# Performance work log

Measured on AMD Instinct MI355X. Metric: run time of the kernel, lower is better.

The kernel has to match this reference:

```python
import jax, jax.numpy as jnp
import numpy as np

N = 100_000
E = 1_600_000
IN_F, E_F, OUT_F = 32, 16, 32


def _glorot(key, shape):
    lim = np.sqrt(6.0 / (shape[0] + shape[1])).astype(np.float32)
    return jax.random.uniform(key, shape, jnp.float32, -lim, lim)


def setup_inputs() -> dict:
    key = jax.random.key(0)
    ks = jax.random.split(key, 12)
    return {
        'h_feat': jax.random.normal(ks[0], (N, IN_F), jnp.float32),
        'e_feat': jax.random.normal(ks[1], (N, E_F), jnp.float32),
        'rain0': jax.random.normal(ks[2], (N,), jnp.float32),
        'w_xx': jax.random.uniform(ks[3], (E,), jnp.float32),
        'w_yy': jax.random.uniform(ks[4], (E,), jnp.float32),
        'W_trans': _glorot(ks[5], (E_F + IN_F, OUT_F)),            # transform_h (no bias)
        'W_rin': _glorot(ks[6], (OUT_F + 4 * E_F, 4 * OUT_F)),     # Rainfall_in (no bias)
        'W_rout': _glorot(ks[7], (4 * OUT_F, 1)),                  # Rainfall_out (no bias)
        'src_xx': jax.random.randint(ks[8], (E,), 0, N, jnp.int32),
        'dst_xx': jax.random.randint(ks[9], (E,), 0, N, jnp.int32),
        'src_yy': jax.random.randint(ks[10], (E,), 0, N, jnp.int32),
        'dst_yy': jax.random.randint(ks[11], (E,), 0, N, jnp.int32),
    }


def _segsum(msg, dst):
    return jax.ops.segment_sum(msg, dst, num_segments=N)


def reference(h_feat, e_feat, rain0, w_xx, w_yy, W_trans, W_rin, W_rout,
              src_xx, dst_xx, src_yy, dst_yy):
    # node-wise transform: cat(h, e) -> linear -> activation_edge (relu)
    emh = jax.nn.relu(jnp.concatenate([h_feat, e_feat], axis=1) @ W_trans)  # [N, OUT_F]
    # copy_u + sum over both edge types, then activation (relu)
    h = jax.nn.relu(_segsum(emh[src_xx], dst_xx) + _segsum(emh[src_yy], dst_yy))
    # first-order weighted differences of e_feat, scattered to dst
    grad_x = _segsum(w_xx[:, None] * (e_feat[src_xx] - e_feat[dst_xx]), dst_xx)  # [N, E_F]
    grad_y = _segsum(w_yy[:, None] * (e_feat[src_yy] - e_feat[dst_yy]), dst_yy)
    # second-order weighted differences
    grad_2x = _segsum(w_xx[:, None] * (grad_x[src_xx] - grad_x[dst_xx]), dst_xx)
    grad_2y = _segsum(w_yy[:, None] * (grad_y[src_yy] - grad_y[dst_yy]), dst_yy)
    h_cat = jnp.concatenate([h, grad_x, grad_y, grad_2x, grad_2y], axis=1)  # [N, OUT_F+4*E_F]
    rain_h = jax.nn.relu(h_cat @ W_rin)
    rainfall = rain0[:, None] + rain_h @ W_rout  # error_mode=True
    return rainfall, h
```

## Files before the change

kernel.cpp:

```cpp
#include <hip/hip_runtime.h>
#include <hip/hip_bf16.h>

#define NN 100000
#define EE 1600000
#define SCAN_CHUNK 4096
#define NB ((NN + SCAN_CHUNK - 1) / SCAN_CHUNK)
#define OFFP (NN + 8)
#define NRANGE 4
#define RSZ (NN / NRANGE)
#define C_CH 16
#define CHUNK_E (EE / C_CH)
#define AP 104

typedef __attribute__((ext_vector_type(8))) short bf16x8;
typedef __attribute__((ext_vector_type(4))) float f32x4;

__device__ inline unsigned short f2bf(float f) {
    unsigned u = __float_as_uint(f);
    return (unsigned short)((u + 0x7FFFu + ((u >> 16) & 1u)) >> 16);
}
__device__ inline float bf2f(unsigned short u) {
    return __uint_as_float(((unsigned)u) << 16);
}

__global__ __launch_bounds__(1024) void fused_th_k(const float* __restrict__ h_feat,
                                                   const float* __restrict__ e_feat,
                                                   const float* __restrict__ W_trans,
                                                   unsigned short* __restrict__ emh_bf,
                                                   unsigned short* __restrict__ ef_bf,
                                                   const int* __restrict__ dst_a,
                                                   const int* __restrict__ dst_b,
                                                   int* __restrict__ partial, int TB) {
    __shared__ float Wl[48 * 32];
    __shared__ int bins[RSZ];
    if ((int)blockIdx.x < TB) {
        for (int i = threadIdx.x; i < 48 * 32; i += 1024) Wl[i] = W_trans[i];
        __syncthreads();
        int t = blockIdx.x * 1024 + threadIdx.x;
        if (t >= NN * 32) return;
        int n = t >> 5, j = t & 31;
        const float* hrow = h_feat + (size_t)n * 32;
        const float* erow = e_feat + (size_t)n * 16;
        float acc = 0.f;
#pragma unroll 8
        for (int k = 0; k < 32; ++k) acc = fmaf(hrow[k], Wl[k * 32 + j], acc);
#pragma unroll 8
        for (int k = 0; k < 16; ++k) acc = fmaf(erow[k], Wl[(32 + k) * 32 + j], acc);
        emh_bf[t] = f2bf(fmaxf(acc, 0.f));
        if (j < 16) ef_bf[(size_t)n * 16 + j] = f2bf(erow[j]);
    } else {
        for (int i = threadIdx.x; i < RSZ; i += 1024) bins[i] = 0;
        __syncthreads();
        const int idx = (int)blockIdx.x - TB;
        const int q = idx & 7;
        const int t = q >> 2;
        const int p = q & 3;
        const int c = idx >> 3;
        const int* dst = t ? dst_b : dst_a;
        const int lo = p * RSZ;
        const long base = (long)c * CHUNK_E;
        for (int i = threadIdx.x * 4; i < CHUNK_E; i += 4096) {
            int4 d = *reinterpret_cast<const int4*>(dst + base + i);
            int x;
            x = d.x - lo; if ((unsigned)x < RSZ) atomicAdd(&bins[x], 1);
            x = d.y - lo; if ((unsigned)x < RSZ) atomicAdd(&bins[x], 1);
            x = d.z - lo; if ((unsigned)x < RSZ) atomicAdd(&bins[x], 1);
            x = d.w - lo; if ((unsigned)x < RSZ) atomicAdd(&bins[x], 1);
        }
        __syncthreads();
        int* pout = partial + (long)(t * C_CH + c) * NN + lo;
        for (int i = threadIdx.x; i < RSZ; i += 1024) pout[i] = bins[i];
    }
}

__global__ __launch_bounds__(1024) void scanA_k(const int* __restrict__ partial,
                                                int* __restrict__ bsum) {
    __shared__ int wsum[16];
    const int b = blockIdx.x;
    const int t = (b >= NB) ? 1 : 0;
    const int i0 = (b % NB) * SCAN_CHUNK + threadIdx.x * 4;
    int4 s = make_int4(0, 0, 0, 0);
    if (i0 < NN) {
#pragma unroll
        for (int c = 0; c < C_CH; ++c) {
            int4 v = *reinterpret_cast<const int4*>(partial + (long)(t * C_CH + c) * NN + i0);
            s.x += v.x; s.y += v.y; s.z += v.z; s.w += v.w;
        }
    }
    int tot = s.x + s.y + s.z + s.w;
#pragma unroll
    for (int d = 32; d; d >>= 1) tot += __shfl_down(tot, d);
    int lane = threadIdx.x & 63, w = threadIdx.x >> 6;
    if (lane == 0) wsum[w] = tot;
    __syncthreads();
    if (threadIdx.x == 0) {
        int sm = 0;
#pragma unroll
        for (int q = 0; q < 16; ++q) sm += wsum[q];
        bsum[b] = sm;
    }
}

__global__ __launch_bounds__(64) void scanB_k(const int* __restrict__ bsum,
                                              int* __restrict__ bbase,
                                              int* __restrict__ off_a,
                                              int* __restrict__ off_b) {
    int lane = threadIdx.x;
    int v = (lane < 2 * NB) ? bsum[lane] : 0;
    int seg = lane / NB;
    int inc = v;
#pragma unroll
    for (int d = 1; d < 64; d <<= 1) {
        int x = __shfl_up(inc, d);
        if (lane >= d && (lane - d) / NB == seg) inc += x;
    }
    int excl = inc - v;
    if (lane < 2 * NB) bbase[lane] = excl;
    if (lane == NB - 1) off_a[NN] = inc;
    if (lane == 2 * NB - 1) off_b[NN] = inc;
}

__global__ __launch_bounds__(1024) void scanC_k(int* __restrict__ partial,
                                                int* __restrict__ off_a,
                                                int* __restrict__ off_b,
                                                const int* __restrict__ bbase) {
    __shared__ int wsum[16];
    const int b = blockIdx.x;
    const int t = (b >= NB) ? 1 : 0;
    int* off = t ? off_b : off_a;
    const int base0 = bbase[b];
    const int i0 = (b % NB) * SCAN_CHUNK + threadIdx.x * 4;
    int4 s = make_int4(0, 0, 0, 0);
    if (i0 < NN) {
#pragma unroll
        for (int c = 0; c < C_CH; ++c) {
            int4 v = *reinterpret_cast<const int4*>(partial + (long)(t * C_CH + c) * NN + i0);
            s.x += v.x; s.y += v.y; s.z += v.z; s.w += v.w;
        }
    }
    int s1 = s.x, s2 = s1 + s.y, s3 = s2 + s.z, tot = s3 + s.w;
    int lane = threadIdx.x & 63, w = threadIdx.x >> 6;
    int inc = tot;
#pragma unroll
    for (int d = 1; d < 64; d <<= 1) {
        int x = __shfl_up(inc, d);
        if (lane >= d) inc += x;
    }
    if (lane == 63) wsum[w] = inc;
    int texcl = inc - tot;
    __syncthreads();
    if (threadIdx.x == 0) {
        int r = 0;
#pragma unroll
        for (int q = 0; q < 16; ++q) { int x = wsum[q]; wsum[q] = r; r += x; }
    }
    __syncthreads();
    const int base = base0 + wsum[w] + texcl;
    if (i0 < NN) {
        *reinterpret_cast<int4*>(off + i0) = make_int4(base, base + s1, base + s2, base + s3);
        int4 run = make_int4(base, base + s1, base + s2, base + s3);
#pragma unroll
        for (int c = 0; c < C_CH; ++c) {
            int* p = partial + (long)(t * C_CH + c) * NN + i0;
            int4 v = *reinterpret_cast<const int4*>(p);
            *reinterpret_cast<int4*>(p) = run;
            run.x += v.x; run.y += v.y; run.z += v.z; run.w += v.w;
        }
    }
}

__global__ __launch_bounds__(1024) void scatter_k(const int* __restrict__ dst_a,
                                                  const int* __restrict__ src_a,
                                                  const float* __restrict__ w_a,
                                                  const int* __restrict__ dst_b,
                                                  const int* __restrict__ src_b,
                                                  const float* __restrict__ w_b,
                                                  const int* __restrict__ partial,
                                                  int2* __restrict__ csr_a,
                                                  int2* __restrict__ csr_b) {
    __shared__ int curs[RSZ];
    const int bid = blockIdx.x;
    const int q = bid & 7;
    const int t = q >> 2;
    const int p = q & 3;
    const int c = bid >> 3;
    const int* dst = t ? dst_b : dst_a;
    const int* src = t ? src_b : src_a;
    const float* wv = t ? w_b : w_a;
    int2* csr = t ? csr_b : csr_a;
    const int lo = p * RSZ;
    const int* pin = partial + (long)(t * C_CH + c) * NN + lo;
    for (int i = threadIdx.x; i < RSZ; i += 1024) curs[i] = pin[i];
    __syncthreads();
    const long base = (long)c * CHUNK_E;
    for (int i = threadIdx.x * 4; i < CHUNK_E; i += 4096) {
        int4 d = *reinterpret_cast<const int4*>(dst + base + i);
        int4 s = *reinterpret_cast<const int4*>(src + base + i);
        float4 w = *reinterpret_cast<const float4*>(wv + base + i);
        int x;
        x = d.x - lo;
        if ((unsigned)x < RSZ) {
            int pp = atomicAdd(&curs[x], 1);
            csr[pp] = make_int2(s.x, __float_as_int(w.x));
        }
        x = d.y - lo;
        if ((unsigned)x < RSZ) {
            int pp = atomicAdd(&curs[x], 1);
            csr[pp] = make_int2(s.y, __float_as_int(w.y));
        }
        x = d.z - lo;
        if ((unsigned)x < RSZ) {
            int pp = atomicAdd(&curs[x], 1);
            csr[pp] = make_int2(s.z, __float_as_int(w.z));
        }
        x = d.w - lo;
        if ((unsigned)x < RSZ) {
            int pp = atomicAdd(&curs[x], 1);
            csr[pp] = make_int2(s.w, __float_as_int(w.w));
        }
    }
}

__global__ __launch_bounds__(256) void pull1_k(const unsigned short* __restrict__ emh_bf,
                                               const unsigned short* __restrict__ ef_bf,
                                               const float* __restrict__ e_feat,
                                               const int2* __restrict__ csr_a,
                                               const int* __restrict__ off_a,
                                               const int2* __restrict__ csr_b,
                                               const int* __restrict__ off_b,
                                               float* __restrict__ out_h,
                                               float* __restrict__ gx,
                                               float* __restrict__ gy,
                                               unsigned short* __restrict__ gx_bf,
                                               unsigned short* __restrict__ gy_bf) {
    int g = blockIdx.x * 256 + threadIdx.x;
    int n = g >> 5, j = g & 31;
    if (n >= NN) return;
    float acc_h = 0.f;

#pragma unroll
    for (int half = 0; half < 2; ++half) {
        const int2* csr = half ? csr_b : csr_a;
        const int* off = half ? off_b : off_a;
        float* gout = half ? gy : gx;
        unsigned short* gbf = half ? gy_bf : gx_bf;
        float acc_g = 0.f, sumw = 0.f;
        int k = off[n], e2 = off[n + 1];
        for (; k + 3 < e2; k += 4) {
            int2 s0 = csr[k], s1 = csr[k + 1], s2 = csr[k + 2], s3 = csr[k + 3];
            float m0 = bf2f(emh_bf[(size_t)s0.x * 32 + j]);
            float m1 = bf2f(emh_bf[(size_t)s1.x * 32 + j]);
            float m2 = bf2f(emh_bf[(size_t)s2.x * 32 + j]);
            float m3 = bf2f(emh_bf[(size_t)s3.x * 32 + j]);
            acc_h += (m0 + m1) + (m2 + m3);
            if (j < 16) {
                float w0 = __int_as_float(s0.y), w1 = __int_as_float(s1.y);
                float w2 = __int_as_float(s2.y), w3 = __int_as_float(s3.y);
                acc_g = fmaf(w0, bf2f(ef_bf[(size_t)s0.x * 16 + j]), acc_g);
                acc_g = fmaf(w1, bf2f(ef_bf[(size_t)s1.x * 16 + j]), acc_g);
                acc_g = fmaf(w2, bf2f(ef_bf[(size_t)s2.x * 16 + j]), acc_g);
                acc_g = fmaf(w3, bf2f(ef_bf[(size_t)s3.x * 16 + j]), acc_g);
                sumw += (w0 + w1) + (w2 + w3);
            }
        }
        for (; k < e2; ++k) {
            int2 s0 = csr[k];
            acc_h += bf2f(emh_bf[(size_t)s0.x * 32 + j]);
            if (j < 16) {
                float w0 = __int_as_float(s0.y);
                acc_g = fmaf(w0, bf2f(ef_bf[(size_t)s0.x * 16 + j]), acc_g);
                sumw += w0;
            }
        }
        if (j < 16) {
            float val = acc_g - sumw * e_feat[(size_t)n * 16 + j];
            gout[(size_t)n * 16 + j] = val;
            gbf[(size_t)n * 16 + j] = f2bf(val);
        }
    }
    out_h[(size_t)n * 32 + j] = fmaxf(acc_h, 0.f);
}

__global__ __launch_bounds__(256) void pull2_k(const float* __restrict__ gx,
                                               const float* __restrict__ gy,
                                               const unsigned short* __restrict__ gx_bf,
                                               const unsigned short* __restrict__ gy_bf,
                                               const int2* __restrict__ csr_a,
                                               const int* __restrict__ off_a,
                                               const int2* __restrict__ csr_b,
                                               const int* __restrict__ off_b,
                                               float* __restrict__ g2x,
                                               float* __restrict__ g2y) {
    int g = blockIdx.x * 256 + threadIdx.x;
    int n = g >> 4, j = g & 15;
    if (n >= NN) return;

#pragma unroll
    for (int half = 0; half < 2; ++half) {
        const int2* csr = half ? csr_b : csr_a;
        const int* off = half ? off_b : off_a;
        const float* gin = half ? gy : gx;
        const unsigned short* gbf = half ? gy_bf : gx_bf;
        float* g2 = half ? g2y : g2x;
        float acc = 0.f, sumw = 0.f;
        int k = off[n], e2 = off[n + 1];
        for (; k + 3 < e2; k += 4) {
            int2 s0 = csr[k], s1 = csr[k + 1], s2 = csr[k + 2], s3 = csr[k + 3];
            float w0 = __int_as_float(s0.y), w1 = __int_as_float(s1.y);
            float w2 = __int_as_float(s2.y), w3 = __int_as_float(s3.y);
            acc = fmaf(w0, bf2f(gbf[(size_t)s0.x * 16 + j]), acc);
            acc = fmaf(w1, bf2f(gbf[(size_t)s1.x * 16 + j]), acc);
            acc = fmaf(w2, bf2f(gbf[(size_t)s2.x * 16 + j]), acc);
            acc = fmaf(w3, bf2f(gbf[(size_t)s3.x * 16 + j]), acc);
            sumw += (w0 + w1) + (w2 + w3);
        }
        for (; k < e2; ++k) {
            int2 s0 = csr[k];
            float w0 = __int_as_float(s0.y);
            acc = fmaf(w0, bf2f(gbf[(size_t)s0.x * 16 + j]), acc);
            sumw += w0;
        }
        g2[(size_t)n * 16 + j] = acc - sumw * gin[(size_t)n * 16 + j];
    }
}

__global__ __launch_bounds__(256) void final_mfma_k(const float* __restrict__ h,
                                                    const float* __restrict__ gx,
                                                    const float* __restrict__ gy,
                                                    const float* __restrict__ g2x,
                                                    const float* __restrict__ g2y,
                                                    const float* __restrict__ rain0,
                                                    const float* __restrict__ W_rin,
                                                    const float* __restrict__ W_rout,
                                                    float* __restrict__ out_rain) {
    __shared__ __align__(16) unsigned short Wt[128 * AP];
    __shared__ __align__(16) unsigned short At[64 * AP];
    __shared__ float Wo[128];
    const int tid = threadIdx.x;

    for (int i = tid; i < 3072; i += 256) {
        int k = i >> 5;
        int c = (i & 31) * 4;
        float4 wv = *reinterpret_cast<const float4*>(W_rin + k * 128 + c);
        Wt[(c + 0) * AP + k] = f2bf(wv.x);
        Wt[(c + 1) * AP + k] = f2bf(wv.y);
        Wt[(c + 2) * AP + k] = f2bf(wv.z);
        Wt[(c + 3) * AP + k] = f2bf(wv.w);
    }
    if (tid < 128) Wo[tid] = W_rout[tid];

    {
        int n = tid >> 2, q = tid & 3;
        int node = blockIdx.x * 64 + n;
        float f[24];
#define LD4(di, p) { float4 v_ = *reinterpret_cast<const float4*>(p); \
                     f[di] = v_.x; f[di+1] = v_.y; f[di+2] = v_.z; f[di+3] = v_.w; }
        if (node < NN) {
            if (q == 0) {
                LD4(0,  h + (size_t)node * 32 + 0);
                LD4(4,  h + (size_t)node * 32 + 4);
                LD4(8,  h + (size_t)node * 32 + 8);
                LD4(12, h + (size_t)node * 32 + 12);
                LD4(16, h + (size_t)node * 32 + 16);
                LD4(20, h + (size_t)node * 32 + 20);
            } else if (q == 1) {
                LD4(0,  h + (size_t)node * 32 + 24);
                LD4(4,  h + (size_t)node * 32 + 28);
                LD4(8,  gx + (size_t)node * 16 + 0);
                LD4(12, gx + (size_t)node * 16 + 4);
                LD4(16, gx + (size_t)node * 16 + 8);
                LD4(20, gx + (size_t)node * 16 + 12);
            } else if (q == 2) {
                LD4(0,  gy + (size_t)node * 16 + 0);
                LD4(4,  gy + (size_t)node * 16 + 4);
                LD4(8,  gy + (size_t)node * 16 + 8);
                LD4(12, gy + (size_t)node * 16 + 12);
                LD4(16, g2x + (size_t)node * 16 + 0);
                LD4(20, g2x + (size_t)node * 16 + 4);
            } else {
                LD4(0,  g2x + (size_t)node * 16 + 8);
                LD4(4,  g2x + (size_t)node * 16 + 12);
                LD4(8,  g2y + (size_t)node * 16 + 0);
                LD4(12, g2y + (size_t)node * 16 + 4);
                LD4(16, g2y + (size_t)node * 16 + 8);
                LD4(20, g2y + (size_t)node * 16 + 12);
            }
        } else {
#pragma unroll
            for (int i = 0; i < 24; ++i) f[i] = 0.f;
        }
#undef LD4
        unsigned pk[12];
#pragma unroll
        for (int i = 0; i < 12; ++i)
            pk[i] = (unsigned)f2bf(f[2 * i]) | ((unsigned)f2bf(f[2 * i + 1]) << 16);
        char* dp = (char*)At + n * (AP * 2) + q * 48;
        *reinterpret_cast<uint4*>(dp + 0)  = make_uint4(pk[0], pk[1], pk[2], pk[3]);
        *reinterpret_cast<uint4*>(dp + 16) = make_uint4(pk[4], pk[5], pk[6], pk[7]);
        *reinterpret_cast<uint4*>(dp + 32) = make_uint4(pk[8], pk[9], pk[10], pk[11]);
    }
    __syncthreads();

    const int w = tid >> 6;
    const int l = tid & 63;
    const int col = l & 15;
    const int kg = l >> 4;
    const char* Ab = (const char*)At + (w * 16 + col) * (AP * 2) + kg * 16;
    const char* Bb = (const char*)Wt + col * (AP * 2) + kg * 16;

    f32x4 acc[8];
#pragma unroll
    for (int ct = 0; ct < 8; ++ct) acc[ct] = (f32x4){0.f, 0.f, 0.f, 0.f};

#pragma unroll
    for (int ks = 0; ks < 3; ++ks) {
        bf16x8 af = *reinterpret_cast<const bf16x8*>(Ab + ks * 64);
#pragma unroll
        for (int ct = 0; ct < 8; ++ct) {
            bf16x8 bfr = *reinterpret_cast<const bf16x8*>(Bb + ct * 16 * (AP * 2) + ks * 64);
            acc[ct] = __builtin_amdgcn_mfma_f32_16x16x32_bf16(af, bfr, acc[ct], 0, 0, 0);
        }
    }

    float s0 = 0.f, s1 = 0.f, s2 = 0.f, s3 = 0.f;
#pragma unroll
    for (int ct = 0; ct < 8; ++ct) {
        float wo = Wo[ct * 16 + col];
        s0 = fmaf(fmaxf(acc[ct][0], 0.f), wo, s0);
        s1 = fmaf(fmaxf(acc[ct][1], 0.f), wo, s1);
        s2 = fmaf(fmaxf(acc[ct][2], 0.f), wo, s2);
        s3 = fmaf(fmaxf(acc[ct][3], 0.f), wo, s3);
    }
#pragma unroll
    for (int m = 1; m < 16; m <<= 1) {
        s0 += __shfl_xor(s0, m);
        s1 += __shfl_xor(s1, m);
        s2 += __shfl_xor(s2, m);
        s3 += __shfl_xor(s3, m);
    }
    if (col == 0) {
        int row = blockIdx.x * 64 + w * 16 + kg * 4;
        if (row + 0 < NN) out_rain[row + 0] = rain0[row + 0] + s0;
        if (row + 1 < NN) out_rain[row + 1] = rain0[row + 1] + s1;
        if (row + 2 < NN) out_rain[row + 2] = rain0[row + 2] + s2;
        if (row + 3 < NN) out_rain[row + 3] = rain0[row + 3] + s3;
    }
}

extern "C" void kernel_launch(void* const* d_in, const int* in_sizes, int n_in,
                              void* d_out, int out_size, void* d_ws, size_t ws_size,
                              hipStream_t stream) {
    const float* h_feat  = (const float*)d_in[0];
    const float* e_feat  = (const float*)d_in[1];
    const float* rain0   = (const float*)d_in[2];
    const float* w_xx    = (const float*)d_in[3];
    const float* w_yy    = (const float*)d_in[4];
    const float* W_trans = (const float*)d_in[5];
    const float* W_rin   = (const float*)d_in[6];
    const float* W_rout  = (const float*)d_in[7];
    const int* src_xx    = (const int*)d_in[8];
    const int* dst_xx    = (const int*)d_in[9];
    const int* src_yy    = (const int*)d_in[10];
    const int* dst_yy    = (const int*)d_in[11];

    unsigned short* emh_bf = (unsigned short*)d_ws;
    unsigned short* ef_bf  = emh_bf + (size_t)NN * 32;
    unsigned short* gx_bf  = ef_bf + (size_t)NN * 16;
    unsigned short* gy_bf  = gx_bf + (size_t)NN * 16;
    float* gx = (float*)(gy_bf + (size_t)NN * 16);
    float* gy = gx + (size_t)NN * 16;
    int2* csr_xx = (int2*)(gy + (size_t)NN * 16);
    int2* csr_yy = csr_xx + EE;
    int* off_xx  = (int*)(csr_yy + EE);
    int* off_yy  = off_xx + OFFP;
    int* partial = off_yy + OFFP;
    float* g2x   = (float*)partial;
    float* g2y   = g2x + (size_t)NN * 16;
    int* bsum    = partial + (size_t)2 * C_CH * NN;
    int* bbase   = bsum + 64;

    float* out_rain = (float*)d_out;
    float* out_h    = out_rain + NN;

    const int TB = (NN * 32 + 1023) / 1024;
    const int HB = 2 * NRANGE * C_CH;
    fused_th_k<<<TB + HB, 1024, 0, stream>>>(h_feat, e_feat, W_trans, emh_bf, ef_bf,
                                             dst_xx, dst_yy, partial, TB);

    scanA_k<<<2 * NB, 1024, 0, stream>>>(partial, bsum);
    scanB_k<<<1, 64, 0, stream>>>(bsum, bbase, off_xx, off_yy);
    scanC_k<<<2 * NB, 1024, 0, stream>>>(partial, off_xx, off_yy, bbase);

    scatter_k<<<2 * NRANGE * C_CH, 1024, 0, stream>>>(
        dst_xx, src_xx, w_xx, dst_yy, src_yy, w_yy, partial, csr_xx, csr_yy);

    pull1_k<<<(NN * 32 + 255) / 256, 256, 0, stream>>>(
        emh_bf, ef_bf, e_feat, csr_xx, off_xx, csr_yy, off_yy,
        out_h, gx, gy, gx_bf, gy_bf);

    pull2_k<<<(NN * 16 + 255) / 256, 256, 0, stream>>>(
        gx, gy, gx_bf, gy_bf, csr_xx, off_xx, csr_yy, off_yy, g2x, g2y);

    final_mfma_k<<<(NN + 63) / 64, 256, 0, stream>>>(
        out_h, gx, gy, g2x, g2y, rain0, W_rin, W_rout, out_rain);
}
```

Before: 301.5 us.

## Replace range-filtered CSR scatter with two-pass bucketed radix partition

Builds the CSR with a two-pass bucket sort. A new count kernel histograms destinations into 1024-node buckets per chunk, a small prefix kernel derives per-chunk bucket cursors, a partition kernel writes packed (src, local dst, weight) records into an intermediate buffer, and a per-bucket kernel scatters them into the final CSR using shared-memory cursors. The old scatter had every block scan its whole chunk four times, once per destination range, and write to scattered global positions. The new scheme reads each edge once per pass and keeps the final scatter local to each bucket. The cost is an extra intermediate buffer, two more launches, and an extra read and write of the edge records. Packing the source index into 20 bits relies on N being below about 1M.

```diff
diff --git a/kernel.cpp b/kernel.cpp
--- a/kernel.cpp
+++ b/kernel.cpp
@@ -10,6 +10,10 @@
 #define RSZ (NN / NRANGE)
 #define C_CH 16
 #define CHUNK_E (EE / C_CH)
+#define BS 1024
+#define NBUK ((NN + BS - 1) / BS)
+#define P_CH 128
+#define PCHUNK_E (EE / P_CH)
 #define AP 104
 
 typedef __attribute__((ext_vector_type(8))) short bf16x8;
@@ -120,7 +124,7 @@
     if (lane == 2 * NB - 1) off_b[NN] = inc;
 }
 
-__global__ __launch_bounds__(1024) void scanC_k(int* __restrict__ partial,
+__global__ __launch_bounds__(1024) void scanC_k(const int* __restrict__ partial,
                                                 int* __restrict__ off_a,
                                                 int* __restrict__ off_b,
                                                 const int* __restrict__ bbase) {
@@ -156,68 +160,111 @@
     }
     __syncthreads();
     const int base = base0 + wsum[w] + texcl;
-    if (i0 < NN) {
+    if (i0 < NN)
         *reinterpret_cast<int4*>(off + i0) = make_int4(base, base + s1, base + s2, base + s3);
-        int4 run = make_int4(base, base + s1, base + s2, base + s3);
-#pragma unroll
-        for (int c = 0; c < C_CH; ++c) {
-            int* p = partial + (long)(t * C_CH + c) * NN + i0;
-            int4 v = *reinterpret_cast<const int4*>(p);
-            *reinterpret_cast<int4*>(p) = run;
-            run.x += v.x; run.y += v.y; run.z += v.z; run.w += v.w;
-        }
-    }
-}
-
-__global__ __launch_bounds__(1024) void scatter_k(const int* __restrict__ dst_a,
-                                                  const int* __restrict__ src_a,
-                                                  const float* __restrict__ w_a,
-                                                  const int* __restrict__ dst_b,
-                                                  const int* __restrict__ src_b,
-                                                  const float* __restrict__ w_b,
-                                                  const int* __restrict__ partial,
-                                                  int2* __restrict__ csr_a,
-                                                  int2* __restrict__ csr_b) {
-    __shared__ int curs[RSZ];
-    const int bid = blockIdx.x;
-    const int q = bid & 7;
-    const int t = q >> 2;
-    const int p = q & 3;
-    const int c = bid >> 3;
+}
+
+__global__ __launch_bounds__(256) void count2_k(const int* __restrict__ dst_a,
+                                                const int* __restrict__ dst_b,
+                                                int* __restrict__ count2) {
+    __shared__ int bins[NBUK];
+    for (int i = threadIdx.x; i < NBUK; i += 256) bins[i] = 0;
+    __syncthreads();
+    const int t = blockIdx.x >> 7;
+    const int c = blockIdx.x & 127;
+    const int* dst = t ? dst_b : dst_a;
+    const long base = (long)c * PCHUNK_E;
+    for (int i = threadIdx.x * 4; i < PCHUNK_E; i += 1024) {
+        int4 d = *reinterpret_cast<const int4*>(dst + base + i);
+        atomicAdd(&bins[d.x >> 10], 1);
+        atomicAdd(&bins[d.y >> 10], 1);
+        atomicAdd(&bins[d.z >> 10], 1);
+        atomicAdd(&bins[d.w >> 10], 1);
+    }
+    __syncthreads();
+    int* out = count2 + ((long)t * P_CH + c) * NBUK;
+    for (int i = threadIdx.x; i < NBUK; i += 256) out[i] = bins[i];
+}
+
+__global__ __launch_bounds__(256) void cur2_k(const int* __restrict__ count2,
+                                              const int* __restrict__ off_a,
+                                              const int* __restrict__ off_b,
+                                              int* __restrict__ cur2) {
+    int tid = threadIdx.x;
+    if (tid >= 2 * NBUK) return;
+    int t = tid / NBUK;
+    int b = tid % NBUK;
+    const int* off = t ? off_b : off_a;
+    int run = off[b * BS];
+    for (int c = 0; c < P_CH; ++c) {
+        long idx = ((long)t * P_CH + c) * NBUK + b;
+        int v = count2[idx];
+        cur2[idx] = run;
+        run += v;
+    }
+}
+
+__global__ __launch_bounds__(1024) void part_k(const int* __restrict__ dst_a,
+                                               const int* __restrict__ src_a,
+                                               const float* __restrict__ w_a,
+                                               const int* __restrict__ dst_b,
+                                               const int* __restrict__ src_b,
+                                               const float* __restrict__ w_b,
+                                               const int* __restrict__ cur2,
+                                               int2* __restrict__ inter_a,
+                                               int2* __restrict__ inter_b) {
+    __shared__ int lcur[NBUK];
+    const int t = blockIdx.x >> 7;
+    const int c = blockIdx.x & 127;
     const int* dst = t ? dst_b : dst_a;
     const int* src = t ? src_b : src_a;
     const float* wv = t ? w_b : w_a;
-    int2* csr = t ? csr_b : csr_a;
-    const int lo = p * RSZ;
-    const int* pin = partial + (long)(t * C_CH + c) * NN + lo;
-    for (int i = threadIdx.x; i < RSZ; i += 1024) curs[i] = pin[i];
-    __syncthreads();
-    const long base = (long)c * CHUNK_E;
-    for (int i = threadIdx.x * 4; i < CHUNK_E; i += 4096) {
+    int2* inter = t ? inter_b : inter_a;
+    {
+        const int* cin = cur2 + ((long)t * P_CH + c) * NBUK;
+        for (int i = threadIdx.x; i < NBUK; i += 1024) lcur[i] = cin[i];
+    }
+    __syncthreads();
+    const long base = (long)c * PCHUNK_E;
+    for (int i = threadIdx.x * 4; i < PCHUNK_E; i += 4096) {
         int4 d = *reinterpret_cast<const int4*>(dst + base + i);
         int4 s = *reinterpret_cast<const int4*>(src + base + i);
         float4 w = *reinterpret_cast<const float4*>(wv + base + i);
-        int x;
-        x = d.x - lo;
-        if ((unsigned)x < RSZ) {
-            int pp = atomicAdd(&curs[x], 1);
-            csr[pp] = make_int2(s.x, __float_as_int(w.x));
-        }
-        x = d.y - lo;
-        if ((unsigned)x < RSZ) {
-            int pp = atomicAdd(&curs[x], 1);
-            csr[pp] = make_int2(s.y, __float_as_int(w.y));
-        }
-        x = d.z - lo;
-        if ((unsigned)x < RSZ) {
-            int pp = atomicAdd(&curs[x], 1);
-            csr[pp] = make_int2(s.z, __float_as_int(w.z));
-        }
-        x = d.w - lo;
-        if ((unsigned)x < RSZ) {
-            int pp = atomicAdd(&curs[x], 1);
-            csr[pp] = make_int2(s.w, __float_as_int(w.w));
-        }
+        int pos;
+        pos = atomicAdd(&lcur[d.x >> 10], 1);
+        inter[pos] = make_int2(s.x | ((d.x & 1023) << 20), __float_as_int(w.x));
+        pos = atomicAdd(&lcur[d.y >> 10], 1);
+        inter[pos] = make_int2(s.y | ((d.y & 1023) << 20), __float_as_int(w.y));
+        pos = atomicAdd(&lcur[d.z >> 10], 1);
+        inter[pos] = make_int2(s.z | ((d.z & 1023) << 20), __float_as_int(w.z));
+        pos = atomicAdd(&lcur[d.w >> 10], 1);
+        inter[pos] = make_int2(s.w | ((d.w & 1023) << 20), __float_as_int(w.w));
+    }
+}
+
+__global__ __launch_bounds__(1024) void scat2_k(const int2* __restrict__ inter_a,
+                                                const int2* __restrict__ inter_b,
+                                                const int* __restrict__ off_a,
+                                                const int* __restrict__ off_b,
+                                                int2* __restrict__ csr_a,
+                                                int2* __restrict__ csr_b) {
+    __shared__ int curs[BS];
+    const int t = ((int)blockIdx.x >= NBUK) ? 1 : 0;
+    const int b = (int)blockIdx.x - t * NBUK;
+    const int2* inter = t ? inter_b : inter_a;
+    const int* off = t ? off_b : off_a;
+    int2* csr = t ? csr_b : csr_a;
+    const int n0 = b * BS;
+    const int nend = (n0 + BS < NN) ? n0 + BS : NN;
+    for (int i = threadIdx.x; i < nend - n0; i += 1024) curs[i] = off[n0 + i];
+    __syncthreads();
+    const int lo = off[n0];
+    const int hi = off[nend];
+    for (int i = lo + threadIdx.x; i < hi; i += 1024) {
+        int2 e = inter[i];
+        int dloc = (e.x >> 20) & 1023;
+        int pos = atomicAdd(&curs[dloc], 1);
+        csr[pos] = make_int2(e.x & 0xFFFFF, e.y);
     }
 }
 
@@ -474,10 +521,15 @@
     int* off_xx  = (int*)(csr_yy + EE);
     int* off_yy  = off_xx + OFFP;
     int* partial = off_yy + OFFP;
-    float* g2x   = (float*)partial;
+    int2* inter_xx = (int2*)partial;
+    int2* inter_yy = inter_xx + EE;
+    float* g2x   = (float*)inter_xx;
     float* g2y   = g2x + (size_t)NN * 16;
-    int* bsum    = partial + (size_t)2 * C_CH * NN;
+    int* tail    = (int*)(inter_yy + EE);
+    int* bsum    = tail;
     int* bbase   = bsum + 64;
+    int* count2  = bbase + 64;
+    int* cur2    = count2 + 2 * P_CH * NBUK;
 
     float* out_rain = (float*)d_out;
     float* out_h    = out_rain + NN;
@@ -491,8 +543,14 @@
     scanB_k<<<1, 64, 0, stream>>>(bsum, bbase, off_xx, off_yy);
     scanC_k<<<2 * NB, 1024, 0, stream>>>(partial, off_xx, off_yy, bbase);
 
-    scatter_k<<<2 * NRANGE * C_CH, 1024, 0, stream>>>(
-        dst_xx, src_xx, w_xx, dst_yy, src_yy, w_yy, partial, csr_xx, csr_yy);
+    count2_k<<<2 * P_CH, 256, 0, stream>>>(dst_xx, dst_yy, count2);
+    cur2_k<<<1, 256, 0, stream>>>(count2, off_xx, off_yy, cur2);
+
+    part_k<<<2 * P_CH, 1024, 0, stream>>>(
+        dst_xx, src_xx, w_xx, dst_yy, src_yy, w_yy, cur2, inter_xx, inter_yy);
+
+    scat2_k<<<2 * NBUK, 1024, 0, stream>>>(
+        inter_xx, inter_yy, off_xx, off_yy, csr_xx, csr_yy);
 
     pull1_k<<<(NN * 32 + 255) / 256, 256, 0, stream>>>(
         emh_bf, ef_bf, e_feat, csr_xx, off_xx, csr_yy, off_yy,
```

Result: faster. 289.8 us (median of 2 runs) (-3.9%).
